# Performance work log

Measured on AMD Instinct MI355X. Metric: run time of the kernel, lower is better.

The kernel has to match this reference:

```python
import jax, jax.numpy as jnp
import numpy as np

B, N, D, E = 8, 512, 64, 32

def setup_inputs() -> dict:
    key = jax.random.key(0)
    k1, k2, k3 = jax.random.split(key, 3)
    x = jax.random.normal(k1, (B, N, D), dtype=jnp.float32)
    We = jax.random.normal(k2, (2 * D, E), dtype=jnp.float32) * (1.0 / np.sqrt(2 * D))
    be = jnp.zeros((E,), dtype=jnp.float32)
    Wr = jax.random.normal(k3, (N * E, 1), dtype=jnp.float32) * (1.0 / np.sqrt(N * E))
    br = jnp.zeros((1,), dtype=jnp.float32)
    return {"x": x, "We": We, "be": be, "Wr": Wr, "br": br}

def reference(x, We, be, Wr, br):
    b, n, d = x.shape
    # cat([x_i, x_j]) @ We == x_i @ We[:d] + x_j @ We[d:]  (avoids materializing the concat)
    W_src, W_dst = We[:d], We[d:]
    src = jnp.einsum('bid,de->bie', x, W_src)   # [B,N,E] contribution of start node i
    dst = jnp.einsum('bjd,de->bje', x, W_dst)   # [B,N,E] contribution of terminal node j
    edges = jax.nn.relu(src[:, :, None, :] + dst[:, None, :, :] + be)  # [B,N,N,E] edge (i->j)
    incoming = jnp.swapaxes(edges, 1, 2)        # [B, N(dst), N(src), E] permute(0,2,1,3)
    agg = incoming.reshape(b, n, n * edges.shape[-1])  # [B,N,N*E]
    delta = agg @ Wr + br                       # [B,N,1]
    return delta
```

## Files before the change

### kernel.cpp

```cpp
#include <hip/hip_runtime.h>

#define BNE (4096 * 32)

__global__ __launch_bounds__(64) void proj_kernel(
    const float* __restrict__ x, const float* __restrict__ We,
    const float* __restrict__ be, const float* __restrict__ br,
    float* __restrict__ out, float* __restrict__ ws)
{
    const int lane = threadIdx.x;
    const int row  = blockIdx.x;
    const int proj = lane >> 5;
    const int e    = lane & 31;

    const float* __restrict__ xrow = x + (size_t)row * 64;
    const float* __restrict__ wcol = We + proj * (64 * 32) + e;

    float acc = 0.0f;
    #pragma unroll
    for (int d = 0; d < 64; ++d)
        acc = fmaf(xrow[d], wcol[d * 32], acc);

    if (proj == 0) acc += be[e];

    ws[(size_t)proj * BNE + (size_t)row * 32 + e] = acc;

    if (blockIdx.x < 64) out[blockIdx.x * 64 + lane] = br[0];
}

__global__ __launch_bounds__(256) void edge_kernel(
    const float* __restrict__ ws, const float* __restrict__ Wr,
    float* __restrict__ out)
{
    const float* __restrict__ src = ws;
    const float* __restrict__ dst = ws + BNE;

    const int b  = blockIdx.z;
    const int j0 = threadIdx.x;
    const int j1 = threadIdx.x + 256;
    const int i0 = blockIdx.x * 8;

    float d0[32], d1[32];
    const float4* __restrict__ dp0 = (const float4*)(dst + ((size_t)(b * 512 + j0)) * 32);
    const float4* __restrict__ dp1 = (const float4*)(dst + ((size_t)(b * 512 + j1)) * 32);
    #pragma unroll
    for (int k = 0; k < 8; ++k) {
        ((float4*)d0)[k] = dp0[k];
        ((float4*)d1)[k] = dp1[k];
    }

    float a00 = 0.f, a01 = 0.f, a10 = 0.f, a11 = 0.f;

    #pragma unroll 2
    for (int ii = 0; ii < 8; ++ii) {
        const int i = i0 + ii;
        const float* __restrict__ srow = src + ((size_t)(b * 512 + i)) * 32;
        const float* __restrict__ wrow = Wr + (size_t)i * 32;
        #pragma unroll
        for (int e = 0; e < 32; e += 2) {
            const float s0 = srow[e],  s1 = srow[e + 1];
            const float w0 = wrow[e],  w1 = wrow[e + 1];
            a00 = fmaf(fmaxf(s0 + d0[e],     0.f), w0, a00);
            a01 = fmaf(fmaxf(s1 + d0[e + 1], 0.f), w1, a01);
            a10 = fmaf(fmaxf(s0 + d1[e],     0.f), w0, a10);
            a11 = fmaf(fmaxf(s1 + d1[e + 1], 0.f), w1, a11);
        }
    }

    atomicAdd(&out[b * 512 + j0], a00 + a01);
    atomicAdd(&out[b * 512 + j1], a10 + a11);
}

extern "C" void kernel_launch(void* const* d_in, const int* in_sizes, int n_in,
                              void* d_out, int out_size, void* d_ws, size_t ws_size,
                              hipStream_t stream) {
    const float* x  = (const float*)d_in[0];
    const float* We = (const float*)d_in[1];
    const float* be = (const float*)d_in[2];
    const float* Wr = (const float*)d_in[3];
    const float* br = (const float*)d_in[4];
    float* out = (float*)d_out;
    float* ws  = (float*)d_ws;

    proj_kernel<<<4096, 64, 0, stream>>>(x, We, be, br, out, ws);
    edge_kernel<<<dim3(64, 1, 8), 256, 0, stream>>>(ws, Wr, out);
}
```

Baseline: 73.24 us.

## Store projections and Wr in fp16 and use packed half add/relu in edge kernel

The projection kernel now writes src/dst projections and a converted copy of Wr as fp16 into the workspace, and processes four rows per 256-thread block with x staged in shared memory. The edge kernel computes src+dst and relu with packed half2 ops, then accumulates in fp32. It uses one j per thread with 512-thread blocks and 16 i rows per block. This halves the memory and register footprint and doubles ALU throughput for the add/max, at the cost of fp16 rounding error in the edge features and weights.

```diff
diff --git a/kernel.cpp b/kernel.cpp
--- a/kernel.cpp
+++ b/kernel.cpp
@@ -2,72 +2,87 @@
 
 #define BNE (4096 * 32)
 
-__global__ __launch_bounds__(64) void proj_kernel(
+typedef _Float16 h1;
+typedef __attribute__((ext_vector_type(2))) _Float16 h2;
+
+__global__ __launch_bounds__(256) void proj_kernel(
     const float* __restrict__ x, const float* __restrict__ We,
-    const float* __restrict__ be, const float* __restrict__ br,
-    float* __restrict__ out, float* __restrict__ ws)
+    const float* __restrict__ be, const float* __restrict__ Wr,
+    const float* __restrict__ br,
+    float* __restrict__ out, h1* __restrict__ hws)
 {
-    const int lane = threadIdx.x;
-    const int row  = blockIdx.x;
+    __shared__ float xs[4][64];
+    const int t  = threadIdx.x;
+    const int r0 = blockIdx.x << 2;
+
+    xs[t >> 6][t & 63] = x[(size_t)r0 * 64 + t];
+    __syncthreads();
+
+    const int w    = t >> 6;
+    const int lane = t & 63;
     const int proj = lane >> 5;
     const int e    = lane & 31;
 
-    const float* __restrict__ xrow = x + (size_t)row * 64;
     const float* __restrict__ wcol = We + proj * (64 * 32) + e;
-
     float acc = 0.0f;
     #pragma unroll
     for (int d = 0; d < 64; ++d)
-        acc = fmaf(xrow[d], wcol[d * 32], acc);
-
+        acc = fmaf(xs[w][d], wcol[d * 32], acc);
     if (proj == 0) acc += be[e];
 
-    ws[(size_t)proj * BNE + (size_t)row * 32 + e] = acc;
+    hws[(size_t)proj * BNE + (size_t)(r0 + w) * 32 + e] = (h1)acc;
 
-    if (blockIdx.x < 64) out[blockIdx.x * 64 + lane] = br[0];
+    if (blockIdx.x < 16) {
+        const int idx = (blockIdx.x << 8) + t;
+        out[idx] = br[0];
+        const float4 wv = ((const float4*)Wr)[idx];
+        h1* __restrict__ wh = hws + 2 * (size_t)BNE + (size_t)idx * 4;
+        wh[0] = (h1)wv.x; wh[1] = (h1)wv.y; wh[2] = (h1)wv.z; wh[3] = (h1)wv.w;
+    }
 }
 
-__global__ __launch_bounds__(256) void edge_kernel(
-    const float* __restrict__ ws, const float* __restrict__ Wr,
-    float* __restrict__ out)
+__global__ __launch_bounds__(512) void edge_kernel(
+    const h1* __restrict__ hws, float* __restrict__ out)
 {
-    const float* __restrict__ src = ws;
-    const float* __restrict__ dst = ws + BNE;
+    const h1* __restrict__ src = hws;
+    const h1* __restrict__ dst = hws + BNE;
+    const h1* __restrict__ wr  = hws + 2 * (size_t)BNE;
 
     const int b  = blockIdx.z;
-    const int j0 = threadIdx.x;
-    const int j1 = threadIdx.x + 256;
-    const int i0 = blockIdx.x * 8;
+    const int j  = threadIdx.x;
+    const int i0 = blockIdx.x << 4;
 
-    float d0[32], d1[32];
-    const float4* __restrict__ dp0 = (const float4*)(dst + ((size_t)(b * 512 + j0)) * 32);
-    const float4* __restrict__ dp1 = (const float4*)(dst + ((size_t)(b * 512 + j1)) * 32);
+    union { float4 f4[4]; h2 d[16]; } u;
+    const float4* __restrict__ dp =
+        (const float4*)(dst + ((size_t)(b * 512 + j)) * 32);
     #pragma unroll
-    for (int k = 0; k < 8; ++k) {
-        ((float4*)d0)[k] = dp0[k];
-        ((float4*)d1)[k] = dp1[k];
-    }
+    for (int k = 0; k < 4; ++k) u.f4[k] = dp[k];
 
-    float a00 = 0.f, a01 = 0.f, a10 = 0.f, a11 = 0.f;
+    const h2 hzero = { (h1)0, (h1)0 };
+    float a0 = 0.f, a1 = 0.f, a2 = 0.f, a3 = 0.f;
 
-    #pragma unroll 2
-    for (int ii = 0; ii < 8; ++ii) {
+    #pragma unroll 4
+    for (int ii = 0; ii < 16; ++ii) {
         const int i = i0 + ii;
-        const float* __restrict__ srow = src + ((size_t)(b * 512 + i)) * 32;
-        const float* __restrict__ wrow = Wr + (size_t)i * 32;
+        const h2* __restrict__ srow =
+            (const h2*)(src + ((size_t)(b * 512 + i)) * 32);
+        const h2* __restrict__ wrow =
+            (const h2*)(wr + (size_t)i * 32);
         #pragma unroll
-        for (int e = 0; e < 32; e += 2) {
-            const float s0 = srow[e],  s1 = srow[e + 1];
-            const float w0 = wrow[e],  w1 = wrow[e + 1];
-            a00 = fmaf(fmaxf(s0 + d0[e],     0.f), w0, a00);
-            a01 = fmaf(fmaxf(s1 + d0[e + 1], 0.f), w1, a01);
-            a10 = fmaf(fmaxf(s0 + d1[e],     0.f), w0, a10);
-            a11 = fmaf(fmaxf(s1 + d1[e + 1], 0.f), w1, a11);
+        for (int e2 = 0; e2 < 16; ++e2) {
+            const h2 s  = srow[e2];
+            const h2 wv = wrow[e2];
+            const h2 tt = __builtin_elementwise_max(s + u.d[e2], hzero);
+            if (e2 & 1) {
+                a2 = fmaf((float)tt.x, (float)wv.x, a2);
+                a3 = fmaf((float)tt.y, (float)wv.y, a3);
+            } else {
+                a0 = fmaf((float)tt.x, (float)wv.x, a0);
+                a1 = fmaf((float)tt.y, (float)wv.y, a1);
+            }
         }
     }
-
-    atomicAdd(&out[b * 512 + j0], a00 + a01);
-    atomicAdd(&out[b * 512 + j1], a10 + a11);
+    atomicAdd(&out[b * 512 + j], (a0 + a1) + (a2 + a3));
 }
 
 extern "C" void kernel_launch(void* const* d_in, const int* in_sizes, int n_in,
@@ -79,8 +94,8 @@
     const float* Wr = (const float*)d_in[3];
     const float* br = (const float*)d_in[4];
     float* out = (float*)d_out;
-    float* ws  = (float*)d_ws;
+    h1* hws = (h1*)d_ws;
 
-    proj_kernel<<<4096, 64, 0, stream>>>(x, We, be, br, out, ws);
-    edge_kernel<<<dim3(64, 1, 8), 256, 0, stream>>>(ws, Wr, out);
+    proj_kernel<<<1024, 256, 0, stream>>>(x, We, be, Wr, br, out, hws);
+    edge_kernel<<<dim3(32, 1, 8), 512, 0, stream>>>(hws, out);
 }
```

Result: no change. 73.52 us (+0.4%).

## Fuse projection and edge kernels into one cooperative kernel with grid sync

Applied to the files above, without the earlier changes.

Merges the projection and edge-aggregation kernels into a single cooperative launch of 256 blocks of 512 threads, with a grid-wide barrier between the two phases. Each block stages 16 rows of x in shared memory and computes their projections. It then handles 16 source rows for one batch, with one destination column per thread. This removes a kernel launch and the inter-kernel gap, at the cost of the grid sync and a different work decomposition (one j per thread, 16 i per block). That decomposition halves per-thread register reuse of the src and Wr loads.

```diff
diff --git a/kernel.cpp b/kernel.cpp
--- a/kernel.cpp
+++ b/kernel.cpp
@@ -1,73 +1,77 @@
 #include <hip/hip_runtime.h>
+#include <hip/hip_cooperative_groups.h>
+
+namespace cg = cooperative_groups;
 
 #define BNE (4096 * 32)
 
-__global__ __launch_bounds__(64) void proj_kernel(
+__global__ __launch_bounds__(512) void fused_kernel(
     const float* __restrict__ x, const float* __restrict__ We,
-    const float* __restrict__ be, const float* __restrict__ br,
-    float* __restrict__ out, float* __restrict__ ws)
+    const float* __restrict__ be, const float* __restrict__ Wr,
+    const float* __restrict__ br, float* __restrict__ out,
+    float* __restrict__ ws)
 {
-    const int lane = threadIdx.x;
-    const int row  = blockIdx.x;
-    const int proj = lane >> 5;
-    const int e    = lane & 31;
+    __shared__ float xs[16 * 64];
+    const int t   = threadIdx.x;
+    const int blk = blockIdx.x;
 
-    const float* __restrict__ xrow = x + (size_t)row * 64;
-    const float* __restrict__ wcol = We + proj * (64 * 32) + e;
+    {
+        const int r0 = blk << 4;
+        const float* __restrict__ xp = x + (size_t)r0 * 64;
+        xs[t]       = xp[t];
+        xs[t + 512] = xp[t + 512];
+        __syncthreads();
 
-    float acc = 0.0f;
-    #pragma unroll
-    for (int d = 0; d < 64; ++d)
-        acc = fmaf(xrow[d], wcol[d * 32], acc);
+        const int w    = t >> 6;
+        const int lane = t & 63;
+        const int proj = lane >> 5;
+        const int e    = lane & 31;
+        const float* __restrict__ wcol = We + proj * (64 * 32) + e;
 
-    if (proj == 0) acc += be[e];
+        #pragma unroll
+        for (int rr = 0; rr < 2; ++rr) {
+            const int lr = 2 * w + rr;
+            float acc = 0.f;
+            #pragma unroll
+            for (int d = 0; d < 64; ++d)
+                acc = fmaf(xs[lr * 64 + d], wcol[d * 32], acc);
+            if (proj == 0) acc += be[e];
+            ws[(size_t)proj * BNE + (size_t)(r0 + lr) * 32 + e] = acc;
+        }
 
-    ws[(size_t)proj * BNE + (size_t)row * 32 + e] = acc;
+        if (blk < 8) out[(blk << 9) + t] = br[0];
+    }
 
-    if (blockIdx.x < 64) out[blockIdx.x * 64 + lane] = br[0];
-}
+    cg::this_grid().sync();
 
-__global__ __launch_bounds__(256) void edge_kernel(
-    const float* __restrict__ ws, const float* __restrict__ Wr,
-    float* __restrict__ out)
-{
     const float* __restrict__ src = ws;
     const float* __restrict__ dst = ws + BNE;
+    const int b  = blk >> 5;
+    const int i0 = (blk & 31) << 4;
+    const int j  = t;
 
-    const int b  = blockIdx.z;
-    const int j0 = threadIdx.x;
-    const int j1 = threadIdx.x + 256;
-    const int i0 = blockIdx.x * 8;
+    float dreg[32];
+    const float4* __restrict__ dp =
+        (const float4*)(dst + ((size_t)((b << 9) + j)) * 32);
+    #pragma unroll
+    for (int k = 0; k < 8; ++k) ((float4*)dreg)[k] = dp[k];
 
-    float d0[32], d1[32];
-    const float4* __restrict__ dp0 = (const float4*)(dst + ((size_t)(b * 512 + j0)) * 32);
-    const float4* __restrict__ dp1 = (const float4*)(dst + ((size_t)(b * 512 + j1)) * 32);
-    #pragma unroll
-    for (int k = 0; k < 8; ++k) {
-        ((float4*)d0)[k] = dp0[k];
-        ((float4*)d1)[k] = dp1[k];
-    }
-
-    float a00 = 0.f, a01 = 0.f, a10 = 0.f, a11 = 0.f;
+    float a0 = 0.f, a1 = 0.f, a2 = 0.f, a3 = 0.f;
 
     #pragma unroll 2
-    for (int ii = 0; ii < 8; ++ii) {
+    for (int ii = 0; ii < 16; ++ii) {
         const int i = i0 + ii;
-        const float* __restrict__ srow = src + ((size_t)(b * 512 + i)) * 32;
+        const float* __restrict__ srow = src + ((size_t)((b << 9) + i)) * 32;
         const float* __restrict__ wrow = Wr + (size_t)i * 32;
         #pragma unroll
-        for (int e = 0; e < 32; e += 2) {
-            const float s0 = srow[e],  s1 = srow[e + 1];
-            const float w0 = wrow[e],  w1 = wrow[e + 1];
-            a00 = fmaf(fmaxf(s0 + d0[e],     0.f), w0, a00);
-            a01 = fmaf(fmaxf(s1 + d0[e + 1], 0.f), w1, a01);
-            a10 = fmaf(fmaxf(s0 + d1[e],     0.f), w0, a10);
-            a11 = fmaf(fmaxf(s1 + d1[e + 1], 0.f), w1, a11);
+        for (int e = 0; e < 32; e += 4) {
+            a0 = fmaf(fmaxf(srow[e]     + dreg[e],     0.f), wrow[e],     a0);
+            a1 = fmaf(fmaxf(srow[e + 1] + dreg[e + 1], 0.f), wrow[e + 1], a1);
+            a2 = fmaf(fmaxf(srow[e + 2] + dreg[e + 2], 0.f), wrow[e + 2], a2);
+            a3 = fmaf(fmaxf(srow[e + 3] + dreg[e + 3], 0.f), wrow[e + 3], a3);
         }
     }
-
-    atomicAdd(&out[b * 512 + j0], a00 + a01);
-    atomicAdd(&out[b * 512 + j1], a10 + a11);
+    atomicAdd(&out[(b << 9) + j], (a0 + a1) + (a2 + a3));
 }
 
 extern "C" void kernel_launch(void* const* d_in, const int* in_sizes, int n_in,
@@ -81,6 +85,8 @@
     float* out = (float*)d_out;
     float* ws  = (float*)d_ws;
 
-    proj_kernel<<<4096, 64, 0, stream>>>(x, We, be, br, out, ws);
-    edge_kernel<<<dim3(64, 1, 8), 256, 0, stream>>>(ws, Wr, out);
+    void* args[] = { (void*)&x, (void*)&We, (void*)&be, (void*)&Wr,
+                     (void*)&br, (void*)&out, (void*)&ws };
+    hipLaunchCooperativeKernel(reinterpret_cast<void*>(fused_kernel),
+                               dim3(256), dim3(512), args, 0, stream);
 }
```

New measurement: 112.0 us. +52.9%, slower.
